# Optimization experiments

Measured on AMD Instinct MI355X. Metric: run time of the kernel, lower is better.

The kernel has to match this reference:

```python
import jax, jax.numpy as jnp
import numpy as np

B, N, FEAT, MSG, LINK_H, CLS = 8, 128, 1024, 256, 512, 600
PROP = 2  # propagate_layers


def setup_inputs() -> dict:
    key = jax.random.key(0)
    ks = jax.random.split(key, 16)
    g = lambda k, shape, s=0.02: jax.random.normal(k, shape, dtype=jnp.float32) * s
    inp = {
        'edge_features': g(ks[0], (B, N, N, FEAT), 1.0),
        'node_features': g(ks[1], (B, N, FEAT), 1.0),
        'adj_mat': jnp.zeros((B, N, N), jnp.float32),          # shape placeholder only
        'node_labels': jnp.zeros((B, N, CLS), jnp.float32),    # shape placeholder only
        'human_nums': 64,
        'obj_nums': 64,
        # feature resize linears (Linear(FEAT -> MSG))
        'W_er': g(ks[2], (MSG, FEAT)), 'b_er': jnp.zeros((MSG,), jnp.float32),
        'W_nr': g(ks[3], (MSG, FEAT)), 'b_nr': jnp.zeros((MSG,), jnp.float32),
        # link fun (GraphConv): 1x1 Conv2d(MSG->LINK_H), ReLU, 1x1 Conv2d(LINK_H->1)
        'W_l1': g(ks[4], (LINK_H, MSG)), 'b_l1': jnp.zeros((LINK_H,), jnp.float32),
        'W_l2': g(ks[5], (1, LINK_H)), 'b_l2': jnp.zeros((1,), jnp.float32),
        # message fun linear_concat_relu: Linear(node+edge = 2*MSG -> MSG), ReLU
        'W_m': g(ks[6], (MSG, 2 * MSG)), 'b_m': jnp.zeros((MSG,), jnp.float32),
        # GRU(input=MSG, hidden=MSG), single layer single step
        'W_ih': g(ks[7], (3 * MSG, MSG)), 'b_ih': jnp.zeros((3 * MSG,), jnp.float32),
        'W_hh': g(ks[8], (3 * MSG, MSG)), 'b_hh': jnp.zeros((3 * MSG,), jnp.float32),
        # readout fc: Linear(MSG -> CLS)
        'W_r': g(ks[9], (CLS, MSG)), 'b_r': jnp.zeros((CLS,), jnp.float32),
    }
    return inp


def reference(edge_features, node_features, adj_mat, node_labels,
              human_nums, obj_nums,
              W_er, b_er, W_nr, b_nr, W_l1, b_l1, W_l2, b_l2,
              W_m, b_m, W_ih, b_ih, W_hh, b_hh, W_r, b_r):
    # valid_node_num = human_nums + obj_nums == N for every batch element.
    # Resize raw features to message size.
    e = edge_features @ W_er.T + b_er        # [B, v, w, MSG]
    h = node_features @ W_nr.T + b_nr        # [B, w, MSG]  (node states are never rewritten in source)
    # Split concat-linear into two matmuls to avoid materializing [B,N,N,2*MSG].
    W_mh, W_me = W_m[:, :MSG], W_m[:, MSG:]
    msg_h = jnp.einsum('bwd,md->bwm', h, W_mh)                 # node part, shared over target v
    msg_e = jnp.einsum('bvwd,md->bvwm', e, W_me) + b_m          # edge part (original e, constant over rounds)
    edge_state = e
    m = None
    pred_adj = None
    for _ in range(PROP):
        # link fun: per-(v,w) MLP over channels (1x1 convs)
        x = jax.nn.relu(edge_state @ W_l1.T + b_l1)             # [B,v,w,LINK_H]
        pred_adj = (x @ W_l2.T + b_l2)[..., 0]                  # [B,N,N]
        sig = jax.nn.sigmoid(pred_adj)
        # message fun linear_concat_relu, gated by predicted adjacency
        m = jax.nn.relu(msg_h[:, None, :, :] + msg_e)           # [B,v,w,MSG]
        m = sig[..., None] * m
        # hidden_edge_states[round+1][:, :, w, v] = m_v[:, :, w]
        edge_state = jnp.swapaxes(m, 1, 2)
    # node update happens per node each round but hidden node states are never
    # written back in the source, so only the last round's GRU step matters.
    m_sum = m.sum(axis=2)                                       # [B,v,MSG]
    gi = m_sum @ W_ih.T + b_ih
    gh = h @ W_hh.T + b_hh
    ir, iz, inn = jnp.split(gi, 3, axis=-1)
    hr, hz, hn = jnp.split(gh, 3, axis=-1)
    r = jax.nn.sigmoid(ir + hr)
    z = jax.nn.sigmoid(iz + hz)
    n = jnp.tanh(inn + r * hn)
    h_new = (1.0 - z) * n + z * h                               # [B,N,MSG]
    pred_node_labels = h_new @ W_r.T + b_r                      # [B,N,CLS]
    return pred_adj, pred_node_labels
```

## Files before the change

### kernel.cpp

```cpp
#include <hip/hip_runtime.h>
#include <cstdint>
#include <cstddef>

#define NND   128
#define FEATD 1024
#define MSGD  256
#define LHD   512
#define CLSD  600
#define LDST  264

typedef __bf16 bf16_t;
typedef bf16_t bf16x8 __attribute__((ext_vector_type(8)));
typedef float  f32x4  __attribute__((ext_vector_type(4)));
typedef unsigned short u16;
typedef u16 u16x8 __attribute__((ext_vector_type(8)));
typedef u16 u16x4 __attribute__((ext_vector_type(4)));

static __device__ __forceinline__ float bf2f(u16 u) {
  union { unsigned u; float f; } x; x.u = ((unsigned)u) << 16; return x.f;
}
static __device__ __forceinline__ u16 f2bf(float f) {
  union { float f; unsigned u; } x; x.f = f;
  return (u16)((x.u + 0x7fffu + ((x.u >> 16) & 1u)) >> 16);
}
static __device__ __forceinline__ f32x4 mfma16(u16x8 a, u16x8 b, f32x4 c) {
  return __builtin_amdgcn_mfma_f32_16x16x32_bf16(
      __builtin_bit_cast(bf16x8, a), __builtin_bit_cast(bf16x8, b), c, 0, 0, 0);
}
static __device__ __forceinline__ f32x4 zero4() {
  f32x4 v; v[0] = 0.f; v[1] = 0.f; v[2] = 0.f; v[3] = 0.f; return v;
}
static __device__ __forceinline__ float sigm(float x) { return 1.0f / (1.0f + expf(-x)); }

__global__ __launch_bounds__(256) void k_cvt_all(
    const float* __restrict__ s0, const float* __restrict__ s1, const float* __restrict__ s2,
    const float* __restrict__ s3, const float* __restrict__ s4, const float* __restrict__ s5,
    u16* __restrict__ d0, u16* __restrict__ d1, u16* __restrict__ d2,
    u16* __restrict__ d3, u16* __restrict__ d4, u16* __restrict__ d5) {
  const int b = blockIdx.x;
  const float* src; u16* dst; int off;
  if (b < 256)      { src = s0; dst = d0; off = b; }
  else if (b < 384) { src = s1; dst = d1; off = b - 256; }
  else if (b < 512) { src = s2; dst = d2; off = b - 384; }
  else if (b < 704) { src = s3; dst = d3; off = b - 512; }
  else if (b < 896) { src = s4; dst = d4; off = b - 704; }
  else              { src = s5; dst = d5; off = b - 896; }
  const int i = off * 1024 + threadIdx.x * 4;
  float4 f = *(const float4*)(src + i);
  u16x4 o; o[0] = f2bf(f.x); o[1] = f2bf(f.y); o[2] = f2bf(f.z); o[3] = f2bf(f.w);
  *(u16x4*)(dst + i) = o;
}

__global__ __launch_bounds__(256) void k_comb(const float* __restrict__ Wm,
                                              const float* __restrict__ Wer,
                                              const float* __restrict__ b_er,
                                              const float* __restrict__ b_m,
                                              u16* __restrict__ WcombB,
                                              float* __restrict__ bcomb) {
  const int m = blockIdx.x >> 2, ch = blockIdx.x & 3;
  const int d = ch * 256 + threadIdx.x;
  float s = 0.f;
  for (int k = 0; k < 256; ++k)
    s += Wm[(size_t)m * 512 + 256 + k] * Wer[(size_t)k * FEATD + d];
  WcombB[(size_t)m * FEATD + d] = f2bf(s);
  if (ch == 0 && threadIdx.x == 0) {
    float bb2 = b_m[m];
    for (int k = 0; k < 256; ++k) bb2 += Wm[(size_t)m * 512 + 256 + k] * b_er[k];
    bcomb[m] = bb2;
  }
}

__global__ __launch_bounds__(256) void s1_hmsg4(const float* __restrict__ node,
                                                const float* __restrict__ Wnr,
                                                const float* __restrict__ bnr,
                                                const float* __restrict__ Wm,
                                                float* __restrict__ h32,
                                                u16* __restrict__ msghB) {
  __shared__ __align__(16) float nrow[4][FEATD];
  __shared__ __align__(16) float hrow[4][MSGD];
  const int r0 = blockIdx.x * 4;
  const int tid = threadIdx.x, lane = tid & 63, wave = tid >> 6;
#pragma unroll
  for (int i = 0; i < 4; ++i)
    *(float4*)(&nrow[i][tid * 4]) = *(const float4*)(node + (size_t)(r0 + i) * FEATD + tid * 4);
  __syncthreads();
  for (int i = 0; i < 64; ++i) {
    const int col = wave * 64 + i;
    const float* wp = Wnr + (size_t)col * FEATD + lane * 16;
    float4 w[4];
#pragma unroll
    for (int j = 0; j < 4; ++j) w[j] = *(const float4*)(wp + j * 4);
    float s[4];
#pragma unroll
    for (int r = 0; r < 4; ++r) {
      const float* np = &nrow[r][lane * 16];
      float a = 0.f;
#pragma unroll
      for (int j = 0; j < 4; ++j) {
        float4 n4 = *(const float4*)(np + j * 4);
        a += w[j].x * n4.x + w[j].y * n4.y + w[j].z * n4.z + w[j].w * n4.w;
      }
      s[r] = a;
    }
#pragma unroll
    for (int off = 1; off < 64; off <<= 1)
#pragma unroll
      for (int r = 0; r < 4; ++r) s[r] += __shfl_xor(s[r], off, 64);
    if (lane == 0) {
      float be = bnr[col];
#pragma unroll
      for (int r = 0; r < 4; ++r) hrow[r][col] = s[r] + be;
    }
  }
  __syncthreads();
#pragma unroll
  for (int i = 0; i < 4; ++i) h32[(size_t)(r0 + i) * MSGD + tid] = hrow[i][tid];
  for (int i = 0; i < 64; ++i) {
    const int col = wave * 64 + i;
    float4 w4 = *(const float4*)(Wm + (size_t)col * 512 + lane * 4);
    float s[4];
#pragma unroll
    for (int r = 0; r < 4; ++r) {
      float4 h4 = *(const float4*)(&hrow[r][lane * 4]);
      s[r] = w4.x * h4.x + w4.y * h4.y + w4.z * h4.z + w4.w * h4.w;
    }
#pragma unroll
    for (int off = 1; off < 64; off <<= 1)
#pragma unroll
      for (int r = 0; r < 4; ++r) s[r] += __shfl_xor(s[r], off, 64);
    if (lane == 0) {
#pragma unroll
      for (int r = 0; r < 4; ++r) msghB[(size_t)(r0 + r) * MSGD + col] = f2bf(s[r]);
    }
  }
}

__global__ __launch_bounds__(256, 2) void k_main_full(
    const float* __restrict__ edge, const u16* __restrict__ Wer, const u16* __restrict__ Wm,
    const u16* __restrict__ Wl1, const float* __restrict__ b_er, const float* __restrict__ b_m,
    const float* __restrict__ b_l1, const float* __restrict__ W_l2, const float* __restrict__ b_l2,
    const u16* __restrict__ msgh, u16* __restrict__ M0g, float* __restrict__ pa_out) {
  __shared__ __align__(16) u16 lsE[64][LDST];
  __shared__ __align__(16) u16 lsM[64][LDST];
  __shared__ float lsPA[4][64];
  __shared__ float lsSig[64];

  const int tid = threadIdx.x, lane = tid & 63, wave = tid >> 6;
  const int lh = lane & 15, lq = lane >> 4;
  const int base = blockIdx.x * 64;
  const int bb = base >> 14, vv = (base >> 7) & 127, w0 = base & 127;

  f32x4 acc[4][4];
#pragma unroll
  for (int m = 0; m < 4; ++m)
#pragma unroll
    for (int t = 0; t < 4; ++t) acc[m][t] = zero4();

  const int srow = tid >> 2;
  const int scq  = (tid & 3) * 16;
  const float* esrc = edge + (size_t)(base + srow) * FEATD + scq;
  float4 lda[4], ldb[4];
  u16x8 bst[2][4];

  auto LOADS_A = [&](int s) {
#pragma unroll
    for (int i = 0; i < 4; ++i) lda[i] = *(const float4*)(esrc + s * 64 + i * 4);
  };
  auto LOADS_B = [&](int s) {
#pragma unroll
    for (int i = 0; i < 4; ++i) ldb[i] = *(const float4*)(esrc + s * 64 + i * 4);
  };
  auto WRITES = [&](const float4* ld, int slot) {
    u16* wp = &lsE[srow][slot * 64 + scq];
    u16x8 o0, o1;
    o0[0] = f2bf(ld[0].x); o0[1] = f2bf(ld[0].y); o0[2] = f2bf(ld[0].z); o0[3] = f2bf(ld[0].w);
    o0[4] = f2bf(ld[1].x); o0[5] = f2bf(ld[1].y); o0[6] = f2bf(ld[1].z); o0[7] = f2bf(ld[1].w);
    o1[0] = f2bf(ld[2].x); o1[1] = f2bf(ld[2].y); o1[2] = f2bf(ld[2].z); o1[3] = f2bf(ld[2].w);
    o1[4] = f2bf(ld[3].x); o1[5] = f2bf(ld[3].y); o1[6] = f2bf(ld[3].z); o1[7] = f2bf(ld[3].w);
    *(u16x8*)wp = o0;
    *(u16x8*)(wp + 8) = o1;
  };
  auto BLOAD = [&](int sk) {
#pragma unroll
    for (int ks = 0; ks < 2; ++ks)
#pragma unroll
      for (int t = 0; t < 4; ++t) {
        int col = wave * 64 + t * 16 + lh;
        bst[ks][t] = *(const u16x8*)(Wer + (size_t)col * FEATD + sk * 64 + ks * 32 + lq * 8);
      }
  };
  auto MCOMP = [&](int slot) {
#pragma unroll
    for (int ks = 0; ks < 2; ++ks) {
      u16x8 afr[4];
#pragma unroll
      for (int m = 0; m < 4; ++m)
        afr[m] = *(const u16x8*)(&lsE[16 * m + lh][slot * 64 + ks * 32 + lq * 8]);
#pragma unroll
      for (int t = 0; t < 4; ++t)
#pragma unroll
        for (int m = 0; m < 4; ++m) acc[m][t] = mfma16(afr[m], bst[ks][t], acc[m][t]);
    }
  };

  LOADS_A(0);
  LOADS_B(1);
  for (int s2 = 0; s2 < 16; s2 += 2) {
    WRITES(lda, 0);
    if (s2 + 2 < 16) LOADS_A(s2 + 2);
    BLOAD(s2);
    __syncthreads();
    MCOMP(0);
    WRITES(ldb, 1);
    if (s2 + 3 < 16) LOADS_B(s2 + 3);
    BLOAD(s2 + 1);
    __syncthreads();
    MCOMP(1);
  }
  __syncthreads();
#pragma unroll
  for (int t = 0; t < 4; ++t) {
    int col = wave * 64 + t * 16 + lh;
    float be = b_er[col];
#pragma unroll
    for (int m = 0; m < 4; ++m)
#pragma unroll
      for (int j = 0; j < 4; ++j)
        lsE[16 * m + 4 * lq + j][col] = f2bf(acc[m][t][j] + be);
  }
  __syncthreads();

  float prow[4][4];
#pragma unroll
  for (int m = 0; m < 4; ++m)
#pragma unroll
    for (int j = 0; j < 4; ++j) prow[m][j] = 0.f;
#pragma unroll
  for (int np = 0; np < 2; ++np) {
#pragma unroll
    for (int m = 0; m < 4; ++m)
#pragma unroll
      for (int t = 0; t < 4; ++t) acc[m][t] = zero4();
    u16x8 bcur[4];
#pragma unroll
    for (int t = 0; t < 4; ++t)
      bcur[t] = *(const u16x8*)(Wl1 + (size_t)(wave * 128 + np * 64 + t * 16 + lh) * MSGD + lq * 8);
#pragma unroll
    for (int ks = 0; ks < 8; ++ks) {
      u16x8 bnxt[4];
      if (ks < 7) {
#pragma unroll
        for (int t = 0; t < 4; ++t)
          bnxt[t] = *(const u16x8*)(Wl1 + (size_t)(wave * 128 + np * 64 + t * 16 + lh) * MSGD +
                                    (ks + 1) * 32 + lq * 8);
      }
      u16x8 afr[4];
#pragma unroll
      for (int m = 0; m < 4; ++m) afr[m] = *(const u16x8*)(&lsE[16 * m + lh][ks * 32 + lq * 8]);
#pragma unroll
      for (int t = 0; t < 4; ++t)
#pragma unroll
        for (int m = 0; m < 4; ++m) acc[m][t] = mfma16(afr[m], bcur[t], acc[m][t]);
      if (ks < 7) {
#pragma unroll
        for (int t = 0; t < 4; ++t) bcur[t] = bnxt[t];
      }
    }
#pragma unroll
    for (int t = 0; t < 4; ++t) {
      int col = wave * 128 + np * 64 + t * 16 + lh;
      float bl = b_l1[col], wl = W_l2[col];
#pragma unroll
      for (int m = 0; m < 4; ++m)
#pragma unroll
        for (int j = 0; j < 4; ++j) prow[m][j] += fmaxf(acc[m][t][j] + bl, 0.f) * wl;
    }
  }
#pragma unroll
  for (int off = 1; off < 16; off <<= 1)
#pragma unroll
    for (int m = 0; m < 4; ++m)
#pragma unroll
      for (int j = 0; j < 4; ++j) prow[m][j] += __shfl_xor(prow[m][j], off, 64);
  if (lh == 0) {
#pragma unroll
    for (int m = 0; m < 4; ++m)
#pragma unroll
      for (int j = 0; j < 4; ++j) lsPA[wave][16 * m + 4 * lq + j] = prow[m][j];
  }
  __syncthreads();
  if (tid < 64) {
    float pa1 = lsPA[0][tid] + lsPA[1][tid] + lsPA[2][tid] + lsPA[3][tid] + b_l2[0];
    lsSig[tid] = sigm(pa1);
  }
#pragma unroll
  for (int i = 0; i < 8; ++i) {
    int idx = tid + i * 256;
    int row = idx >> 5;
    int c8 = (idx & 31) << 3;
    *(u16x8*)(&lsM[row][c8]) =
        *(const u16x8*)(msgh + (size_t)(bb * NND + w0 + row) * MSGD + c8);
  }
  __syncthreads();

#pragma unroll
  for (int m = 0; m < 4; ++m)
#pragma unroll
    for (int t = 0; t < 4; ++t) acc[m][t] = zero4();
  {
    u16x8 bcur[4];
#pragma unroll
    for (int t = 0; t < 4; ++t)
      bcur[t] = *(const u16x8*)(Wm + (size_t)(wave * 64 + t * 16 + lh) * 512 + 256 + lq * 8);
#pragma unroll
    for (int ks = 0; ks < 8; ++ks) {
      u16x8 bnxt[4];
      if (ks < 7) {
#pragma unroll
        for (int t = 0; t < 4; ++t)
          bnxt[t] = *(const u16x8*)(Wm + (size_t)(wave * 64 + t * 16 + lh) * 512 + 256 +
                                    (ks + 1) * 32 + lq * 8);
      }
      u16x8 afr[4];
#pragma unroll
      for (int m = 0; m < 4; ++m) afr[m] = *(const u16x8*)(&lsE[16 * m + lh][ks * 32 + lq * 8]);
#pragma unroll
      for (int t = 0; t < 4; ++t)
#pragma unroll
        for (int m = 0; m < 4; ++m) acc[m][t] = mfma16(afr[m], bcur[t], acc[m][t]);
      if (ks < 7) {
#pragma unroll
        for (int t = 0; t < 4; ++t) bcur[t] = bnxt[t];
      }
    }
  }
#pragma unroll
  for (int t = 0; t < 4; ++t) {
    int col = wave * 64 + t * 16 + lh;
    float bm = b_m[col];
#pragma unroll
    for (int m = 0; m < 4; ++m)
#pragma unroll
      for (int j = 0; j < 4; ++j) {
        int row = 16 * m + 4 * lq + j;
        float mh = bf2f(lsM[row][col]);
        lsM[row][col] = f2bf(fmaxf(acc[m][t][j] + bm + mh, 0.f));
      }
  }
  __syncthreads();
#pragma unroll
  for (int i = 0; i < 8; ++i) {
    int idx = tid + i * 256;
    int row = idx >> 5;
    int c8 = (idx & 31) << 3;
    u16x8 m0v = *(const u16x8*)(&lsM[row][c8]);
    if (M0g) *(u16x8*)(M0g + (size_t)(base + row) * MSGD + c8) = m0v;
    float s = lsSig[row];
    u16x8 sc;
#pragma unroll
    for (int j = 0; j < 8; ++j) sc[j] = f2bf(bf2f(m0v[j]) * s);
    *(u16x8*)(&lsM[row][c8]) = sc;
  }
  __syncthreads();

#pragma unroll
  for (int m = 0; m < 4; ++m)
#pragma unroll
    for (int j = 0; j < 4; ++j) prow[m][j] = 0.f;
#pragma unroll
  for (int np = 0; np < 2; ++np) {
#pragma unroll
    for (int m = 0; m < 4; ++m)
#pragma unroll
      for (int t = 0; t < 4; ++t) acc[m][t] = zero4();
    u16x8 bcur[4];
#pragma unroll
    for (int t = 0; t < 4; ++t)
      bcur[t] = *(const u16x8*)(Wl1 + (size_t)(wave * 128 + np * 64 + t * 16 + lh) * MSGD + lq * 8);
#pragma unroll
    for (int ks = 0; ks < 8; ++ks) {
      u16x8 bnxt[4];
      if (ks < 7) {
#pragma unroll
        for (int t = 0; t < 4; ++t)
          bnxt[t] = *(const u16x8*)(Wl1 + (size_t)(wave * 128 + np * 64 + t * 16 + lh) * MSGD +
                                    (ks + 1) * 32 + lq * 8);
      }
      u16x8 afr[4];
#pragma unroll
      for (int m = 0; m < 4; ++m) afr[m] = *(const u16x8*)(&lsM[16 * m + lh][ks * 32 + lq * 8]);
#pragma unroll
      for (int t = 0; t < 4; ++t)
#pragma unroll
        for (int m = 0; m < 4; ++m) acc[m][t] = mfma16(afr[m], bcur[t], acc[m][t]);
      if (ks < 7) {
#pragma unroll
        for (int t = 0; t < 4; ++t) bcur[t] = bnxt[t];
      }
    }
#pragma unroll
    for (int t = 0; t < 4; ++t) {
      int col = wave * 128 + np * 64 + t * 16 + lh;
      float bl = b_l1[col], wl = W_l2[col];
#pragma unroll
      for (int m = 0; m < 4; ++m)
#pragma unroll
        for (int j = 0; j < 4; ++j) prow[m][j] += fmaxf(acc[m][t][j] + bl, 0.f) * wl;
    }
  }
#pragma unroll
  for (int off = 1; off < 16; off <<= 1)
#pragma unroll
    for (int m = 0; m < 4; ++m)
#pragma unroll
      for (int j = 0; j < 4; ++j) prow[m][j] += __shfl_xor(prow[m][j], off, 64);
  if (lh == 0) {
#pragma unroll
    for (int m = 0; m < 4; ++m)
#pragma unroll
      for (int j = 0; j < 4; ++j) lsPA[wave][16 * m + 4 * lq + j] = prow[m][j];
  }
  __syncthreads();
  if (tid < 64) {
    float q = lsPA[0][tid] + lsPA[1][tid] + lsPA[2][tid] + lsPA[3][tid] + b_l2[0];
    size_t o = ((size_t)bb * NND + (w0 + tid)) * NND + vv;
    pa_out[o] = q;
  }
}

__global__ __launch_bounds__(256) void k_msum_lite(const u16* __restrict__ M0g,
                                                   const float* __restrict__ qv,
                                                   float* __restrict__ msum) {
  __shared__ float sig[128];
  __shared__ __align__(16) float part[8][256];
  const int bv = blockIdx.x, tid = threadIdx.x;
  if (tid < 128) sig[tid] = sigm(qv[(size_t)bv * NND + tid]);
  __syncthreads();
  const int cg = (tid & 31) * 8, rg = tid >> 5;
  float a[8];
#pragma unroll
  for (int j = 0; j < 8; ++j) a[j] = 0.f;
  for (int i = 0; i < 16; ++i) {
    int row = rg + i * 8;
    u16x8 v = *(const u16x8*)(M0g + ((size_t)bv * NND + row) * MSGD + cg);
    float s = sig[row];
#pragma unroll
    for (int j = 0; j < 8; ++j) a[j] += s * bf2f(v[j]);
  }
#pragma unroll
  for (int j = 0; j < 8; ++j) part[rg][cg + j] = a[j];
  __syncthreads();
  float r = 0.f;
#pragma unroll
  for (int g = 0; g < 8; ++g) r += part[g][tid];
  msum[(size_t)bv * MSGD + tid] = r;
}

__global__ __launch_bounds__(256, 2) void k_msum2(
    const float* __restrict__ edge, const u16* __restrict__ Wcomb,
    const float* __restrict__ bcomb, const u16* __restrict__ msgh,
    const float* __restrict__ qv, float* __restrict__ msum) {
  __shared__ __align__(16) u16 lsE[64][LDST];
  __shared__ __align__(16) u16 lsM[64][LDST];
  __shared__ float lsSig[64];
  const int tid = threadIdx.x, lane = tid & 63, wave = tid >> 6;
  const int lh = lane & 15, lq = lane >> 4;
  const int bv = blockIdx.x;
  const int bb = bv >> 7;

  float csum[4] = {0.f, 0.f, 0.f, 0.f};

  for (int hh = 0; hh < 2; ++hh) {
    if (tid < 64) lsSig[tid] = sigm(qv[(size_t)bv * NND + hh * 64 + tid]);
#pragma unroll
    for (int i = 0; i < 8; ++i) {
      int idx = tid + i * 256;
      int row = idx >> 5;
      int c8 = (idx & 31) << 3;
      *(u16x8*)(&lsM[row][c8]) =
          *(const u16x8*)(msgh + (size_t)(bb * NND + hh * 64 + row) * MSGD + c8);
    }
    f32x4 acc[4][4];
#pragma unroll
    for (int m = 0; m < 4; ++m)
#pragma unroll
      for (int t = 0; t < 4; ++t) acc[m][t] = zero4();

    for (int kc = 0; kc < 4; ++kc) {
#pragma unroll
      for (int i = 0; i < 16; ++i) {
        int idx = tid + i * 256;
        int row = idx >> 6;
        int c4 = (idx & 63) << 2;
        float4 f = *(const float4*)(edge + (size_t)(bv * NND + hh * 64 + row) * FEATD + kc * 256 + c4);
        u16x4 o; o[0] = f2bf(f.x); o[1] = f2bf(f.y); o[2] = f2bf(f.z); o[3] = f2bf(f.w);
        *(u16x4*)(&lsE[row][c4]) = o;
      }
      __syncthreads();
#pragma unroll
      for (int ks = 0; ks < 8; ++ks) {
        u16x8 afr[4];
#pragma unroll
        for (int m = 0; m < 4; ++m) afr[m] = *(const u16x8*)(&lsE[16 * m + lh][ks * 32 + lq * 8]);
        const int kg = kc * 256 + ks * 32 + lq * 8;
#pragma unroll
        for (int t = 0; t < 4; ++t) {
          int col = wave * 64 + t * 16 + lh;
          u16x8 bfr = *(const u16x8*)(Wcomb + (size_t)col * FEATD + kg);
#pragma unroll
          for (int m = 0; m < 4; ++m) acc[m][t] = mfma16(afr[m], bfr, acc[m][t]);
        }
      }
      __syncthreads();
    }
#pragma unroll
    for (int t = 0; t < 4; ++t) {
      int col = wave * 64 + t * 16 + lh;
      float bc = bcomb[col];
#pragma unroll
      for (int m = 0; m < 4; ++m)
#pragma unroll
        for (int j = 0; j < 4; ++j) {
          int row = 16 * m + 4 * lq + j;
          float m0 = fmaxf(acc[m][t][j] + bc + bf2f(lsM[row][col]), 0.f);
          csum[t] += lsSig[row] * m0;
        }
    }
    __syncthreads();
  }
#pragma unroll
  for (int off = 16; off < 64; off <<= 1)
#pragma unroll
    for (int t = 0; t < 4; ++t) csum[t] += __shfl_xor(csum[t], off, 64);
  if (lq == 0) {
#pragma unroll
    for (int t = 0; t < 4; ++t)
      msum[(size_t)bv * MSGD + wave * 64 + t * 16 + lh] = csum[t];
  }
}

__global__ __launch_bounds__(256) void k_gru_bf(const float* __restrict__ msum,
                                                const float* __restrict__ h32,
                                                const u16* __restrict__ Wih, const float* __restrict__ bih,
                                                const u16* __restrict__ Whh, const float* __restrict__ bhh,
                                                const u16* __restrict__ Wr, const float* __restrict__ br,
                                                float* __restrict__ outlab) {
  __shared__ __align__(16) float sM[8][256];
  __shared__ __align__(16) float sH[8][256];
  __shared__ __align__(16) float sHn[8][256];
  const int tid = threadIdx.x;
  const int r0 = blockIdx.x * 8;
#pragma unroll
  for (int i = 0; i < 2; ++i) {
    int idx = tid + i * 256;
    int row = idx >> 6;
    int c = (idx & 63) << 2;
    *(float4*)(&sM[row][c]) = *(const float4*)(msum + (size_t)(r0 + row) * 256 + c);
    *(float4*)(&sH[row][c]) = *(const float4*)(h32 + (size_t)(r0 + row) * 256 + c);
  }
  __syncthreads();
  float gi[3][8], gh[3][8];
#pragma unroll
  for (int c = 0; c < 3; ++c) {
    float bi_ = bih[tid + 256 * c], bh_ = bhh[tid + 256 * c];
#pragma unroll
    for (int rr = 0; rr < 8; ++rr) { gi[c][rr] = bi_; gh[c][rr] = bh_; }
  }
  for (int k = 0; k < 256; k += 8) {
    u16x8 wi[3], wh[3];
#pragma unroll
    for (int c = 0; c < 3; ++c) {
      wi[c] = *(const u16x8*)(Wih + (size_t)(tid + 256 * c) * 256 + k);
      wh[c] = *(const u16x8*)(Whh + (size_t)(tid + 256 * c) * 256 + k);
    }
#pragma unroll
    for (int j = 0; j < 8; ++j) {
      float wif0 = bf2f(wi[0][j]), wif1 = bf2f(wi[1][j]), wif2 = bf2f(wi[2][j]);
      float whf0 = bf2f(wh[0][j]), whf1 = bf2f(wh[1][j]), whf2 = bf2f(wh[2][j]);
#pragma unroll
      for (int rr = 0; rr < 8; ++rr) {
        float ms = sM[rr][k + j], hh = sH[rr][k + j];
        gi[0][rr] += wif0 * ms; gi[1][rr] += wif1 * ms; gi[2][rr] += wif2 * ms;
        gh[0][rr] += whf0 * hh; gh[1][rr] += whf1 * hh; gh[2][rr] += whf2 * hh;
      }
    }
  }
#pragma unroll
  for (int rr = 0; rr < 8; ++rr) {
    float r = sigm(gi[0][rr] + gh[0][rr]);
    float z = sigm(gi[1][rr] + gh[1][rr]);
    float n = tanhf(gi[2][rr] + r * gh[2][rr]);
    sHn[rr][tid] = (1.f - z) * n + z * sH[rr][tid];
  }
  __syncthreads();
  float lab[3][8];
  int cs[3]; bool has[3];
#pragma unroll
  for (int c = 0; c < 3; ++c) {
    cs[c] = tid + 256 * c;
    has[c] = cs[c] < CLSD;
    float b0 = has[c] ? br[cs[c]] : 0.f;
#pragma unroll
    for (int rr = 0; rr < 8; ++rr) lab[c][rr] = b0;
  }
  u16x8 zv;
#pragma unroll
  for (int j = 0; j < 8; ++j) zv[j] = 0;
  for (int k = 0; k < 256; k += 8) {
    u16x8 wr[3];
#pragma unroll
    for (int c = 0; c < 3; ++c)
      wr[c] = has[c] ? *(const u16x8*)(Wr + (size_t)cs[c] * 256 + k) : zv;
#pragma unroll
    for (int j = 0; j < 8; ++j) {
      float w0 = bf2f(wr[0][j]), w1 = bf2f(wr[1][j]), w2 = bf2f(wr[2][j]);
#pragma unroll
      for (int rr = 0; rr < 8; ++rr) {
        float hv = sHn[rr][k + j];
        lab[0][rr] += w0 * hv; lab[1][rr] += w1 * hv; lab[2][rr] += w2 * hv;
      }
    }
  }
#pragma unroll
  for (int c = 0; c < 3; ++c) {
    if (has[c]) {
#pragma unroll
      for (int rr = 0; rr < 8; ++rr)
        outlab[(size_t)(r0 + rr) * CLSD + cs[c]] = lab[c][rr];
    }
  }
}

extern "C" void kernel_launch(void* const* d_in, const int* in_sizes, int n_in,
                              void* d_out, int out_size, void* d_ws, size_t ws_size,
                              hipStream_t stream) {
  const float* edge = (const float*)d_in[0];
  const float* node = (const float*)d_in[1];
  const float* W_er = (const float*)d_in[6];
  const float* b_er = (const float*)d_in[7];
  const float* W_nr = (const float*)d_in[8];
  const float* b_nr = (const float*)d_in[9];
  const float* W_l1 = (const float*)d_in[10];
  const float* b_l1 = (const float*)d_in[11];
  const float* W_l2 = (const float*)d_in[12];
  const float* b_l2 = (const float*)d_in[13];
  const float* W_m  = (const float*)d_in[14];
  const float* b_m  = (const float*)d_in[15];
  const float* W_ih = (const float*)d_in[16];
  const float* b_ih = (const float*)d_in[17];
  const float* W_hh = (const float*)d_in[18];
  const float* b_hh = (const float*)d_in[19];
  const float* W_r  = (const float*)d_in[20];
  const float* b_r  = (const float*)d_in[21];

  char* ws = (char*)d_ws;
  size_t off = 0;
  auto alloc = [&](size_t bytes) -> void* {
    void* p = ws + off;
    off += (bytes + 511) & ~(size_t)511;
    return p;
  };
  u16* WerB     = (u16*)alloc((size_t)262144 * 2);
  u16* WmB      = (u16*)alloc((size_t)131072 * 2);
  u16* Wl1B     = (u16*)alloc((size_t)131072 * 2);
  u16* WihB     = (u16*)alloc((size_t)196608 * 2);
  u16* WhhB     = (u16*)alloc((size_t)196608 * 2);
  u16* WrB      = (u16*)alloc((size_t)153600 * 2);
  u16* WcombB   = (u16*)alloc((size_t)262144 * 2);
  float* bcombF = (float*)alloc((size_t)256 * 4);
  u16* msghB    = (u16*)alloc((size_t)262144 * 2);
  float* h32    = (float*)alloc((size_t)262144 * 4);
  float* msum   = (float*)alloc((size_t)262144 * 4);
  u16* M0g      = (u16*)alloc((size_t)33554432 * 2);
  size_t off_m0 = off;
  const bool fast = (ws_size >= off_m0);
  u16* M0arg = fast ? M0g : (u16*)nullptr;

  float* out_pa  = (float*)d_out;
  float* out_lab = out_pa + 131072;

  k_cvt_all<<<1046, 256, 0, stream>>>(W_er, W_m, W_l1, W_ih, W_hh, W_r,
                                      WerB, WmB, Wl1B, WihB, WhhB, WrB);
  s1_hmsg4<<<256, 256, 0, stream>>>(node, W_nr, b_nr, W_m, h32, msghB);
  if (!fast)
    k_comb<<<1024, 256, 0, stream>>>(W_m, W_er, b_er, b_m, WcombB, bcombF);

  k_main_full<<<2048, 256, 0, stream>>>(edge, WerB, WmB, Wl1B, b_er, b_m, b_l1, W_l2, b_l2,
                                        msghB, M0arg, out_pa);
  if (fast)
    k_msum_lite<<<1024, 256, 0, stream>>>(M0g, out_pa, msum);
  else
    k_msum2<<<1024, 256, 0, stream>>>(edge, WcombB, bcombF, msghB, out_pa, msum);
  k_gru_bf<<<128, 256, 0, stream>>>(msum, h32, WihB, b_ih, WhhB, b_hh, WrB, b_r, out_lab);
}
```

Measured before the change: 588.6 us.

## Fuse message-sum reduction with GRU and readout; process 8 rows per block

On the fast path, the sigmoid-gated message-sum reduction, the GRU cell update and the readout linear are merged into one kernel. Each block handles 8 (b,v) rows, so the msum buffer round-trip and one kernel launch go away. The node-resize kernel also doubles its rows per block, halving its grid and reusing each weight load across more rows. The trade-off is that the reduction now runs on only 128 blocks instead of 1024, which limits parallelism while streaming the 64MB M0 buffer.

```diff
diff --git a/kernel.cpp b/kernel.cpp
--- a/kernel.cpp
+++ b/kernel.cpp
@@ -70,18 +70,18 @@
   }
 }
 
-__global__ __launch_bounds__(256) void s1_hmsg4(const float* __restrict__ node,
+__global__ __launch_bounds__(256) void s1_hmsg8(const float* __restrict__ node,
                                                 const float* __restrict__ Wnr,
                                                 const float* __restrict__ bnr,
                                                 const float* __restrict__ Wm,
                                                 float* __restrict__ h32,
                                                 u16* __restrict__ msghB) {
-  __shared__ __align__(16) float nrow[4][FEATD];
-  __shared__ __align__(16) float hrow[4][MSGD];
-  const int r0 = blockIdx.x * 4;
+  __shared__ __align__(16) float nrow[8][FEATD];
+  __shared__ __align__(16) float hrow[8][MSGD];
+  const int r0 = blockIdx.x * 8;
   const int tid = threadIdx.x, lane = tid & 63, wave = tid >> 6;
 #pragma unroll
-  for (int i = 0; i < 4; ++i)
+  for (int i = 0; i < 8; ++i)
     *(float4*)(&nrow[i][tid * 4]) = *(const float4*)(node + (size_t)(r0 + i) * FEATD + tid * 4);
   __syncthreads();
   for (int i = 0; i < 64; ++i) {
@@ -90,9 +90,9 @@
     float4 w[4];
 #pragma unroll
     for (int j = 0; j < 4; ++j) w[j] = *(const float4*)(wp + j * 4);
-    float s[4];
-#pragma unroll
-    for (int r = 0; r < 4; ++r) {
+    float s[8];
+#pragma unroll
+    for (int r = 0; r < 8; ++r) {
       const float* np = &nrow[r][lane * 16];
       float a = 0.f;
 #pragma unroll
@@ -105,32 +105,32 @@
 #pragma unroll
     for (int off = 1; off < 64; off <<= 1)
 #pragma unroll
-      for (int r = 0; r < 4; ++r) s[r] += __shfl_xor(s[r], off, 64);
+      for (int r = 0; r < 8; ++r) s[r] += __shfl_xor(s[r], off, 64);
     if (lane == 0) {
       float be = bnr[col];
 #pragma unroll
-      for (int r = 0; r < 4; ++r) hrow[r][col] = s[r] + be;
-    }
-  }
-  __syncthreads();
-#pragma unroll
-  for (int i = 0; i < 4; ++i) h32[(size_t)(r0 + i) * MSGD + tid] = hrow[i][tid];
+      for (int r = 0; r < 8; ++r) hrow[r][col] = s[r] + be;
+    }
+  }
+  __syncthreads();
+#pragma unroll
+  for (int i = 0; i < 8; ++i) h32[(size_t)(r0 + i) * MSGD + tid] = hrow[i][tid];
   for (int i = 0; i < 64; ++i) {
     const int col = wave * 64 + i;
     float4 w4 = *(const float4*)(Wm + (size_t)col * 512 + lane * 4);
-    float s[4];
-#pragma unroll
-    for (int r = 0; r < 4; ++r) {
+    float s[8];
+#pragma unroll
+    for (int r = 0; r < 8; ++r) {
       float4 h4 = *(const float4*)(&hrow[r][lane * 4]);
       s[r] = w4.x * h4.x + w4.y * h4.y + w4.z * h4.z + w4.w * h4.w;
     }
 #pragma unroll
     for (int off = 1; off < 64; off <<= 1)
 #pragma unroll
-      for (int r = 0; r < 4; ++r) s[r] += __shfl_xor(s[r], off, 64);
+      for (int r = 0; r < 8; ++r) s[r] += __shfl_xor(s[r], off, 64);
     if (lane == 0) {
 #pragma unroll
-      for (int r = 0; r < 4; ++r) msghB[(size_t)(r0 + r) * MSGD + col] = f2bf(s[r]);
+      for (int r = 0; r < 8; ++r) msghB[(size_t)(r0 + r) * MSGD + col] = f2bf(s[r]);
     }
   }
 }
@@ -428,32 +428,128 @@
   }
 }
 
-__global__ __launch_bounds__(256) void k_msum_lite(const u16* __restrict__ M0g,
-                                                   const float* __restrict__ qv,
-                                                   float* __restrict__ msum) {
-  __shared__ float sig[128];
+__global__ __launch_bounds__(256) void k_msum_gru(
+    const u16* __restrict__ M0g, const float* __restrict__ qv, const float* __restrict__ h32,
+    const u16* __restrict__ Wih, const float* __restrict__ bih,
+    const u16* __restrict__ Whh, const float* __restrict__ bhh,
+    const u16* __restrict__ Wr, const float* __restrict__ br,
+    float* __restrict__ outlab) {
+  __shared__ __align__(16) float sM[8][256];
+  __shared__ __align__(16) float sH[8][256];
+  __shared__ __align__(16) float sHn[8][256];
   __shared__ __align__(16) float part[8][256];
-  const int bv = blockIdx.x, tid = threadIdx.x;
-  if (tid < 128) sig[tid] = sigm(qv[(size_t)bv * NND + tid]);
-  __syncthreads();
+  __shared__ float sig[8][128];
+  const int tid = threadIdx.x;
+  const int r0 = blockIdx.x * 8;
+
+#pragma unroll
+  for (int i = 0; i < 4; ++i) {
+    int idx = tid + i * 256;
+    int r = idx >> 7, w = idx & 127;
+    sig[r][w] = sigm(qv[(size_t)(r0 + r) * NND + w]);
+  }
+#pragma unroll
+  for (int i = 0; i < 2; ++i) {
+    int idx = tid + i * 256;
+    int row = idx >> 6;
+    int c = (idx & 63) << 2;
+    *(float4*)(&sH[row][c]) = *(const float4*)(h32 + (size_t)(r0 + row) * 256 + c);
+  }
+  __syncthreads();
+
   const int cg = (tid & 31) * 8, rg = tid >> 5;
-  float a[8];
-#pragma unroll
-  for (int j = 0; j < 8; ++j) a[j] = 0.f;
-  for (int i = 0; i < 16; ++i) {
-    int row = rg + i * 8;
-    u16x8 v = *(const u16x8*)(M0g + ((size_t)bv * NND + row) * MSGD + cg);
-    float s = sig[row];
-#pragma unroll
-    for (int j = 0; j < 8; ++j) a[j] += s * bf2f(v[j]);
-  }
-#pragma unroll
-  for (int j = 0; j < 8; ++j) part[rg][cg + j] = a[j];
-  __syncthreads();
-  float r = 0.f;
-#pragma unroll
-  for (int g = 0; g < 8; ++g) r += part[g][tid];
-  msum[(size_t)bv * MSGD + tid] = r;
+  for (int r = 0; r < 8; ++r) {
+    float a[8];
+#pragma unroll
+    for (int j = 0; j < 8; ++j) a[j] = 0.f;
+    const u16* p = M0g + (size_t)(r0 + r) * NND * MSGD;
+    for (int i = 0; i < 16; ++i) {
+      int row = rg + i * 8;
+      u16x8 v = *(const u16x8*)(p + (size_t)row * MSGD + cg);
+      float s = sig[r][row];
+#pragma unroll
+      for (int j = 0; j < 8; ++j) a[j] += s * bf2f(v[j]);
+    }
+#pragma unroll
+    for (int j = 0; j < 8; ++j) part[rg][cg + j] = a[j];
+    __syncthreads();
+    float acc = 0.f;
+#pragma unroll
+    for (int g = 0; g < 8; ++g) acc += part[g][tid];
+    sM[r][tid] = acc;
+    __syncthreads();
+  }
+
+  float gi[3][8], gh[3][8];
+#pragma unroll
+  for (int c = 0; c < 3; ++c) {
+    float bi_ = bih[tid + 256 * c], bh_ = bhh[tid + 256 * c];
+#pragma unroll
+    for (int rr = 0; rr < 8; ++rr) { gi[c][rr] = bi_; gh[c][rr] = bh_; }
+  }
+  for (int k = 0; k < 256; k += 8) {
+    u16x8 wi[3], wh[3];
+#pragma unroll
+    for (int c = 0; c < 3; ++c) {
+      wi[c] = *(const u16x8*)(Wih + (size_t)(tid + 256 * c) * 256 + k);
+      wh[c] = *(const u16x8*)(Whh + (size_t)(tid + 256 * c) * 256 + k);
+    }
+#pragma unroll
+    for (int j = 0; j < 8; ++j) {
+      float wif0 = bf2f(wi[0][j]), wif1 = bf2f(wi[1][j]), wif2 = bf2f(wi[2][j]);
+      float whf0 = bf2f(wh[0][j]), whf1 = bf2f(wh[1][j]), whf2 = bf2f(wh[2][j]);
+#pragma unroll
+      for (int rr = 0; rr < 8; ++rr) {
+        float ms = sM[rr][k + j], hh = sH[rr][k + j];
+        gi[0][rr] += wif0 * ms; gi[1][rr] += wif1 * ms; gi[2][rr] += wif2 * ms;
+        gh[0][rr] += whf0 * hh; gh[1][rr] += whf1 * hh; gh[2][rr] += whf2 * hh;
+      }
+    }
+  }
+#pragma unroll
+  for (int rr = 0; rr < 8; ++rr) {
+    float r = sigm(gi[0][rr] + gh[0][rr]);
+    float z = sigm(gi[1][rr] + gh[1][rr]);
+    float n = tanhf(gi[2][rr] + r * gh[2][rr]);
+    sHn[rr][tid] = (1.f - z) * n + z * sH[rr][tid];
+  }
+  __syncthreads();
+  float lab[3][8];
+  int cs[3]; bool has[3];
+#pragma unroll
+  for (int c = 0; c < 3; ++c) {
+    cs[c] = tid + 256 * c;
+    has[c] = cs[c] < CLSD;
+    float b0 = has[c] ? br[cs[c]] : 0.f;
+#pragma unroll
+    for (int rr = 0; rr < 8; ++rr) lab[c][rr] = b0;
+  }
+  u16x8 zv;
+#pragma unroll
+  for (int j = 0; j < 8; ++j) zv[j] = 0;
+  for (int k = 0; k < 256; k += 8) {
+    u16x8 wr[3];
+#pragma unroll
+    for (int c = 0; c < 3; ++c)
+      wr[c] = has[c] ? *(const u16x8*)(Wr + (size_t)cs[c] * 256 + k) : zv;
+#pragma unroll
+    for (int j = 0; j < 8; ++j) {
+      float w0 = bf2f(wr[0][j]), w1 = bf2f(wr[1][j]), w2 = bf2f(wr[2][j]);
+#pragma unroll
+      for (int rr = 0; rr < 8; ++rr) {
+        float hv = sHn[rr][k + j];
+        lab[0][rr] += w0 * hv; lab[1][rr] += w1 * hv; lab[2][rr] += w2 * hv;
+      }
+    }
+  }
+#pragma unroll
+  for (int c = 0; c < 3; ++c) {
+    if (has[c]) {
+#pragma unroll
+      for (int rr = 0; rr < 8; ++rr)
+        outlab[(size_t)(r0 + rr) * CLSD + cs[c]] = lab[c][rr];
+    }
+  }
 }
 
 __global__ __launch_bounds__(256, 2) void k_msum2(
@@ -681,15 +777,17 @@
 
   k_cvt_all<<<1046, 256, 0, stream>>>(W_er, W_m, W_l1, W_ih, W_hh, W_r,
                                       WerB, WmB, Wl1B, WihB, WhhB, WrB);
-  s1_hmsg4<<<256, 256, 0, stream>>>(node, W_nr, b_nr, W_m, h32, msghB);
+  s1_hmsg8<<<128, 256, 0, stream>>>(node, W_nr, b_nr, W_m, h32, msghB);
   if (!fast)
     k_comb<<<1024, 256, 0, stream>>>(W_m, W_er, b_er, b_m, WcombB, bcombF);
 
   k_main_full<<<2048, 256, 0, stream>>>(edge, WerB, WmB, Wl1B, b_er, b_m, b_l1, W_l2, b_l2,
                                         msghB, M0arg, out_pa);
-  if (fast)
-    k_msum_lite<<<1024, 256, 0, stream>>>(M0g, out_pa, msum);
-  else
+  if (fast) {
+    k_msum_gru<<<128, 256, 0, stream>>>(M0g, out_pa, h32, WihB, b_ih, WhhB, b_hh, WrB, b_r,
+                                        out_lab);
+  } else {
     k_msum2<<<1024, 256, 0, stream>>>(edge, WcombB, bcombF, msghB, out_pa, msum);
-  k_gru_bf<<<128, 256, 0, stream>>>(msum, h32, WihB, b_ih, WhhB, b_hh, WrB, b_r, out_lab);
-}
+    k_gru_bf<<<128, 256, 0, stream>>>(msum, h32, WihB, b_ih, WhhB, b_hh, WrB, b_r, out_lab);
+  }
+}
```

Measured after the change: 669.0 us. +13.7%, slower.
